# Kernel optimization log

Hardware: AMD Instinct MI355X
Metric: run time of the kernel (lower is better)

Reference implementation:

```python
import jax, jax.numpy as jnp
import numpy as np

B_SZ = 4; SEQ = 2048; D_INPUT = 40; D_MODEL = 128; N_LAYERS = 4
D_STATE = 16; EXPAND = 2; D_INNER = D_MODEL * EXPAND
N_HEADS = 4; D_HEAD = D_MODEL // N_HEADS; MAX_LANDMARKS = 100
EPS_RMS = 1.1920929e-07  # torch nn.RMSNorm default eps = finfo(float32).eps
EPS_LN = 1e-5
A_FLOOR = 1e-4


def _rms(x, w):
    return x * jax.lax.rsqrt(jnp.mean(x * x, -1, keepdims=True) + EPS_RMS) * w


def _ln(x, w, b):
    m = jnp.mean(x, -1, keepdims=True)
    v = jnp.mean((x - m) ** 2, -1, keepdims=True)
    return (x - m) * jax.lax.rsqrt(v + EPS_LN) * w + b


def _mamba3_block(xin, Wi, Wx, Wdt, bdt, Alog, Bb, Cb, Bnw, Cnw, rf, Dv, Wo):
    # xin: (B,L,d_model)
    xz = xin @ Wi                       # (B,L,2*d_inner)
    xp, z = jnp.split(xz, 2, axis=-1)
    xp = jax.nn.silu(xp)
    sp = xp @ Wx                        # (B,L,2*d_state+2)
    B_raw = sp[..., :D_STATE]
    C_raw = sp[..., D_STATE:2 * D_STATE]
    dt_in = sp[..., -2:-1]
    lam_in = sp[..., -1:]
    Bm = _rms(B_raw + Bb, Bnw)
    Cm = _rms(C_raw + Cb, Cnw)
    dt = jax.nn.softplus(dt_in @ Wdt + bdt)   # (B,L,d_inner)
    lam = jax.nn.sigmoid(lam_in)              # (B,L,1)
    # data-dependent RoPE on B and C
    freqs = jax.nn.softplus(rf)                                  # (d_state//2,)
    ang = jnp.cumsum(jnp.mean(dt, -1, keepdims=True), axis=1) * freqs  # (B,L,ds/2)
    ca, sa = jnp.cos(ang), jnp.sin(ang)

    def rot(M):
        e, o = M[..., ::2], M[..., 1::2]
        return jnp.stack([e * ca - o * sa, e * sa + o * ca], -1).reshape(M.shape)

    Bm, Cm = rot(Bm), rot(Cm)
    A = jnp.minimum(-jnp.exp(Alog), -A_FLOOR)   # (d_inner,d_state)
    dte = dt[..., None]                          # (B,L,d_inner,1)
    dA = jnp.exp(A * dte)                        # (B,L,d_inner,d_state)
    Bx = Bm[:, :, None, :] * xp[..., None]       # (B,L,d_inner,d_state)
    Bx_prev = jnp.concatenate([jnp.zeros_like(Bx[:, :1]), Bx[:, :-1]], axis=1)
    lame = lam[..., None]                        # (B,L,1,1)
    u = (1.0 - lame) * dte * dA * Bx_prev + lame * dte * Bx
    u = u.at[:, 0].set(dte[:, 0] * Bx[:, 0])     # t==0 case: h = dt*B*x (no lambda)

    def step(h, inp):
        dA_t, u_t, C_t = inp
        h = dA_t * h + u_t
        return h, jnp.sum(h * C_t[:, None, :], -1)

    h0 = jnp.zeros((xin.shape[0], D_INNER, D_STATE), xin.dtype)
    _, ys = jax.lax.scan(step, h0, (jnp.swapaxes(dA, 0, 1), jnp.swapaxes(u, 0, 1), jnp.swapaxes(Cm, 0, 1)))
    y = jnp.swapaxes(ys, 0, 1)                   # (B,L,d_inner)
    y = y + xp * Dv
    y = y * jax.nn.silu(z)
    return y @ Wo


def _landmark_attn(mo, skip, hw, WQ, bQ, WK, bK, WV, bV, WO, bO):
    Bsz, L, Dm = skip.shape
    k = min(MAX_LANDMARKS, L)
    _, idx = jax.lax.top_k(hw, k)
    idx = jnp.sort(idx, axis=1)                            # (B,k)
    kv = jnp.take_along_axis(skip, idx[..., None], axis=1)  # (B,k,Dm)
    q = mo[:, -1:, :]                                       # (B,1,Dm)
    Q = (q @ WQ + bQ).reshape(Bsz, 1, N_HEADS, D_HEAD).transpose(0, 2, 1, 3)
    K = (kv @ WK + bK).reshape(Bsz, k, N_HEADS, D_HEAD).transpose(0, 2, 1, 3)
    V = (kv @ WV + bV).reshape(Bsz, k, N_HEADS, D_HEAD).transpose(0, 2, 1, 3)
    scores = jnp.einsum('bhqd,bhkd->bhqk', Q, K) * (D_HEAD ** -0.5)
    probs = jax.nn.softmax(scores, axis=-1)
    out = jnp.einsum('bhqk,bhkd->bhqd', probs, V).transpose(0, 2, 1, 3).reshape(Bsz, Dm)
    return out @ WO + bO


def setup_inputs() -> dict:
    key = jax.random.key(0)
    ks = iter(jax.random.split(key, 64))

    def nrm(shape, s=0.02):
        return jax.random.normal(next(ks), shape, jnp.float32) * s

    nl, ds, di, dm = N_LAYERS, D_STATE, D_INNER, D_MODEL
    inp = {}
    inp['x'] = jax.random.normal(next(ks), (B_SZ, SEQ, D_INPUT), jnp.float32)
    inp['hawkes_weights'] = jax.random.uniform(next(ks), (B_SZ, SEQ), jnp.float32)
    inp['emb_W'] = nrm((D_INPUT, dm)); inp['emb_b'] = jnp.zeros(dm, jnp.float32)
    inp['skip_W'] = nrm((D_INPUT, dm)); inp['skip_b'] = jnp.zeros(dm, jnp.float32)
    inp['in_proj_W'] = nrm((nl, dm, 2 * di))
    inp['x_proj_W'] = nrm((nl, di, 2 * ds + 2))
    inp['dt_proj_W'] = nrm((nl, 1, di), 1.0)
    inp['dt_proj_b'] = jnp.full((nl, di), -1.0, jnp.float32)
    inp['A_log'] = jnp.broadcast_to(jnp.log(jnp.arange(1, ds + 1, dtype=jnp.float32)), (nl, di, ds)) * jnp.ones((nl, di, ds), jnp.float32)
    inp['B_bias'] = jnp.ones((nl, ds), jnp.float32)
    inp['C_bias'] = jnp.ones((nl, ds), jnp.float32)
    inp['Bn_w'] = jnp.ones((nl, ds), jnp.float32)
    inp['Cn_w'] = jnp.ones((nl, ds), jnp.float32)
    inp['rope_freqs'] = nrm((nl, ds // 2), 0.01)
    inp['D_param'] = jnp.ones((nl, di), jnp.float32)
    inp['out_proj_W'] = nrm((nl, di, dm))
    inp['ln_w'] = jnp.ones((nl, dm), jnp.float32); inp['ln_b'] = jnp.zeros((nl, dm), jnp.float32)
    inp['fn_w'] = jnp.ones(dm, jnp.float32); inp['fn_b'] = jnp.zeros(dm, jnp.float32)
    for nm in ('Q', 'K', 'V', 'O'):
        inp['W' + nm] = nrm((dm, dm)); inp['b' + nm] = jnp.zeros(dm, jnp.float32)
    return inp


def reference(x, hawkes_weights, emb_W, emb_b, skip_W, skip_b, in_proj_W, x_proj_W,
              dt_proj_W, dt_proj_b, A_log, B_bias, C_bias, Bn_w, Cn_w, rope_freqs,
              D_param, out_proj_W, ln_w, ln_b, fn_w, fn_b, WQ, bQ, WK, bK, WV, bV, WO, bO):
    w = hawkes_weights[..., None]
    h = (x @ emb_W + emb_b) * w          # Hawkes-damped embedding for Mamba path
    skip = (x @ skip_W + skip_b) * w     # Hawkes skip for attention KV
    for i in range(N_LAYERS):
        h = h + _mamba3_block(_ln(h, ln_w[i], ln_b[i]), in_proj_W[i], x_proj_W[i],
                              dt_proj_W[i], dt_proj_b[i], A_log[i], B_bias[i], C_bias[i],
                              Bn_w[i], Cn_w[i], rope_freqs[i], D_param[i], out_proj_W[i])
    mo = _ln(h, fn_w, fn_b)
    return _landmark_attn(mo, skip, hawkes_weights, WQ, bQ, WK, bK, WV, bV, WO, bO)
```

## Files before the change

kernel.cpp:

```cpp
#include <hip/hip_runtime.h>
#include <hip/hip_fp16.h>
#include <math.h>

#define BSZ   4
#define SEQL  2048
#define DIN   40
#define DM    128
#define DI    256
#define DS    16
#define NL    4
#define NHEAD 4
#define DHEAD 32
#define KLM   100
#define NC    128
#define TC    16
#define NROWS 8
#define EROWS 16

typedef _Float16 v2h __attribute__((ext_vector_type(2)));

__device__ __forceinline__ float rcp_(float x){ return __builtin_amdgcn_rcpf(x); }
__device__ __forceinline__ float sigmoidf_(float x){ return rcp_(1.0f + __expf(-x)); }
__device__ __forceinline__ float siluf_(float x){ return x*rcp_(1.0f + __expf(-x)); }
__device__ __forceinline__ float softplusf_(float x){ return fmaxf(x,0.0f) + __logf(1.0f + __expf(-fabsf(x))); }
__device__ __forceinline__ float fdot2_(__half2 a, __half2 b, float c){
  return __builtin_amdgcn_fdot2(*(v2h*)&a, *(v2h*)&b, c, false);
}

__device__ __forceinline__ void load8(const float* p, float* r){
  const float4* q = (const float4*)p;
  float4 a=q[0], b=q[1];
  r[0]=a.x;r[1]=a.y;r[2]=a.z;r[3]=a.w; r[4]=b.x;r[5]=b.y;r[6]=b.z;r[7]=b.w;
}
__device__ __forceinline__ void store8(float* p, const float* r){
  float4* q = (float4*)p;
  q[0]=make_float4(r[0],r[1],r[2],r[3]);  q[1]=make_float4(r[4],r[5],r[6],r[7]);
}
__device__ __forceinline__ void load16(const float* p, float* r){
  load8(p, r); load8(p+8, r+8);
}
__device__ __forceinline__ void store16(float* p, const float* r){
  store8(p, r); store8(p+8, r+8);
}

__global__ __launch_bounds__(256) void convw_kernel(
    const float* __restrict__ inW, const float* __restrict__ outW,
    __half* __restrict__ Wip, __half* __restrict__ Woh)
{
  const int i = blockIdx.x*256 + threadIdx.x;
  if (i < NL*DM*2*DI){
    const int col = i & 511;
    const int klin = i >> 9;
    const int l = klin >> 7, k = klin & 127;
    Wip[(((size_t)(l*64 + (k>>1))*512 + col) << 1) + (k & 1)] = __float2half_rn(inW[i]);
  }
  if (i < NL*DI*DM) Woh[i] = __float2half_rn(outW[i]);
}

__global__ __launch_bounds__(256) void topk_kernel(
    const float* __restrict__ hw, int* __restrict__ idxl_g)
{
  __shared__ int redcnt[2][4];
  __shared__ int eqc[8][4], gtc[8][4];

  const int b = blockIdx.x;
  const int t = threadIdx.x;
  const int lane = t & 63, w = t >> 6;

  const float* hwp = hw + (size_t)b*SEQL;
  unsigned vb[8];
  #pragma unroll
  for (int q=0;q<8;q++) vb[q] = __float_as_uint(hwp[q*256 + t]);

  unsigned kth = 0u;
  for (int bit=31; bit>=0; --bit){
    const unsigned cand = kth | (1u << bit);
    int c0 = 0;
    #pragma unroll
    for (int q=0;q<8;q++) c0 += __popcll(__ballot(vb[q] >= cand));
    const int par = bit & 1;
    if (lane == 0) redcnt[par][w] = c0;
    __syncthreads();
    const int tot = redcnt[par][0]+redcnt[par][1]+redcnt[par][2]+redcnt[par][3];
    if (tot >= KLM) kth = cand;
  }

  unsigned long long beq[8], bgt[8];
  #pragma unroll
  for (int q=0;q<8;q++){
    beq[q] = __ballot(vb[q] == kth);
    bgt[q] = __ballot(vb[q] >  kth);
  }
  if (lane == 0){
    #pragma unroll
    for (int q=0;q<8;q++){ eqc[q][w] = __popcll(beq[q]); gtc[q][w] = __popcll(bgt[q]); }
  }
  __syncthreads();
  {
    int gtTot = 0;
    #pragma unroll
    for (int q=0;q<8;q++) gtTot += gtc[q][0]+gtc[q][1]+gtc[q][2]+gtc[q][3];
    const int need_eq = KLM - gtTot;
    const unsigned long long lmask = (lane==0) ? 0ull : ((~0ull) >> (64-lane));
    int eqPfx = 0, gtPfx = 0;
    #pragma unroll
    for (int q=0;q<8;q++){
      int eqWP = 0, gtWP = 0;
      for (int w2=0; w2<w; ++w2){ eqWP += eqc[q][w2]; gtWP += gtc[q][w2]; }
      const int eqBefore = eqPfx + eqWP + __popcll(beq[q] & lmask);
      const int gtBefore = gtPfx + gtWP + __popcll(bgt[q] & lmask);
      if (vb[q] > kth){
        const int pos = gtBefore + min(eqBefore, need_eq);
        if (pos < KLM) idxl_g[b*KLM + pos] = q*256 + t;
      } else if (vb[q] == kth && eqBefore < need_eq){
        const int pos = gtBefore + eqBefore;
        if (pos < KLM) idxl_g[b*KLM + pos] = q*256 + t;
      }
      eqPfx += eqc[q][0]+eqc[q][1]+eqc[q][2]+eqc[q][3];
      gtPfx += gtc[q][0]+gtc[q][1]+gtc[q][2]+gtc[q][3];
    }
  }
}

__global__ __launch_bounds__(256) void embed_kernel(
    const float* __restrict__ x, const float* __restrict__ hw,
    const float* __restrict__ eW, const float* __restrict__ eb,
    const float* __restrict__ sW, const float* __restrict__ sb,
    float* __restrict__ hb, float* __restrict__ sk)
{
  __shared__ float xr[EROWS][DIN];
  const int t = threadIdx.x;
  const size_t R0 = (size_t)blockIdx.x * EROWS;
  for (int e=t; e<EROWS*DIN; e+=256) ((float*)xr)[e] = x[R0*DIN + e];
  __syncthreads();
  const int c = t & (DM-1), g = t >> 7;
  float ae[8], as[8];
  #pragma unroll
  for (int j=0;j<8;j++){ ae[j]=0.0f; as[j]=0.0f; }
  for (int k=0;k<DIN;k++){
    const float we  = eW[(size_t)k*DM + c];
    const float ws_ = sW[(size_t)k*DM + c];
    #pragma unroll
    for (int j=0;j<8;j++){
      const float xv = xr[g*8+j][k];
      ae[j] = fmaf(xv, we, ae[j]);
      as[j] = fmaf(xv, ws_, as[j]);
    }
  }
  const float ebv = eb[c], sbv = sb[c];
  #pragma unroll
  for (int j=0;j<8;j++){
    const size_t R = R0 + g*8 + j;
    const float w = hw[R];
    hb[R*DM + c] = (ae[j]+ebv)*w;
    sk[R*DM + c] = (as[j]+sbv)*w;
  }
}

__global__ __launch_bounds__(256) void pre_kernel(
    const float* __restrict__ hb,
    const __half* __restrict__ Wip, const float* __restrict__ Wx,
    const float* __restrict__ Wdt, const float* __restrict__ bdt,
    const float* __restrict__ Bb, const float* __restrict__ Cb,
    const float* __restrict__ Bnw, const float* __restrict__ Cnw,
    const float* __restrict__ lnw, const float* __restrict__ lnb,
    __half* __restrict__ xph, __half* __restrict__ zsh,
    float* __restrict__ dtin, float* __restrict__ Shalf,
    float* __restrict__ Bmb, float* __restrict__ Cmb,
    float* __restrict__ lamb, float* __restrict__ mdtb)
{
  __shared__ __half2 xinh[NROWS][64+2];
  __shared__ float xps[NROWS][DI+4];
  __shared__ float spl[NROWS][40];
  __shared__ float pr[NROWS][4];

  const int t = threadIdx.x;
  const size_t R0 = (size_t)blockIdx.x * NROWS;

  {
    const int r = t >> 5, j = t & 31;
    const float4 v = ((const float4*)(hb + (R0 + r)*DM))[j];
    float s = v.x+v.y+v.z+v.w;
    #pragma unroll
    for (int o=16;o>0;o>>=1) s += __shfl_xor(s,o,32);
    const float m = s*(1.0f/DM);
    const float dx=v.x-m, dy=v.y-m, dz=v.z-m, dw=v.w-m;
    float ss = dx*dx+dy*dy+dz*dz+dw*dw;
    #pragma unroll
    for (int o=16;o>0;o>>=1) ss += __shfl_xor(ss,o,32);
    const float inv = 1.0f/sqrtf(ss*(1.0f/DM) + 1e-5f);
    const int c = j*4;
    const float v0 = dx*inv*lnw[c+0] + lnb[c+0];
    const float v1 = dy*inv*lnw[c+1] + lnb[c+1];
    const float v2 = dz*inv*lnw[c+2] + lnb[c+2];
    const float v3 = dw*inv*lnw[c+3] + lnb[c+3];
    xinh[r][2*j]   = __halves2half2(__float2half_rn(v0), __float2half_rn(v1));
    xinh[r][2*j+1] = __halves2half2(__float2half_rn(v2), __float2half_rn(v3));
  }
  __syncthreads();

  {
    float2 a[NROWS];
    #pragma unroll
    for (int r=0;r<NROWS;r++){ a[r].x=0.0f; a[r].y=0.0f; }
    const __half2* Wc = (const __half2*)Wip + 2*t;
    #pragma unroll 4
    for (int p=0;p<64;p++){
      const float2 wv = *(const float2*)&Wc[(size_t)p*512];
      const __half2 w0 = *(const __half2*)&wv.x;
      const __half2 w1 = *(const __half2*)&wv.y;
      #pragma unroll
      for (int r=0;r<NROWS;r++){
        const __half2 xv = xinh[r][p];
        a[r].x = fdot2_(xv, w0, a[r].x);
        a[r].y = fdot2_(xv, w1, a[r].y);
      }
    }
    if (t < 128){
      #pragma unroll
      for (int r=0;r<NROWS;r++){
        const float sx = siluf_(a[r].x), sy = siluf_(a[r].y);
        xps[r][2*t] = sx; xps[r][2*t+1] = sy;
        *(__half2*)&xph[(R0+r)*DI + 2*t] =
            __halves2half2(__float2half_rn(sx), __float2half_rn(sy));
      }
    } else {
      const int zc = 2*t - 2*DI + DI;
      #pragma unroll
      for (int r=0;r<NROWS;r++){
        const float sx = siluf_(a[r].x), sy = siluf_(a[r].y);
        *(__half2*)&zsh[(R0+r)*DI + zc] =
            __halves2half2(__float2half_rn(sx), __float2half_rn(sy));
      }
    }
  }
  __syncthreads();

  if (t < 136){
    const int r = t & 7, op = t >> 3;
    float ax=0.0f, ay=0.0f;
    for (int k=0;k<DI;k+=4){
      const float4 xv = *(const float4*)&xps[r][k];
      const float2 w0 = *(const float2*)&Wx[(size_t)(k+0)*34 + 2*op];
      const float2 w1 = *(const float2*)&Wx[(size_t)(k+1)*34 + 2*op];
      const float2 w2 = *(const float2*)&Wx[(size_t)(k+2)*34 + 2*op];
      const float2 w3 = *(const float2*)&Wx[(size_t)(k+3)*34 + 2*op];
      ax = fmaf(xv.x,w0.x,ax); ay = fmaf(xv.x,w0.y,ay);
      ax = fmaf(xv.y,w1.x,ax); ay = fmaf(xv.y,w1.y,ay);
      ax = fmaf(xv.z,w2.x,ax); ay = fmaf(xv.z,w2.y,ay);
      ax = fmaf(xv.w,w3.x,ax); ay = fmaf(xv.w,w3.y,ay);
    }
    spl[r][2*op] = ax; spl[r][2*op+1] = ay;
  }
  __syncthreads();

  {
    const int half = t >> 7;
    const int r2 = (t >> 4) & 7, s2 = t & 15;
    const float* bias = half ? Cb : Bb;
    const float* wn   = half ? Cnw : Bnw;
    const float v = spl[r2][half*DS + s2] + bias[s2];
    float ss = v*v;
    #pragma unroll
    for (int o=8;o>0;o>>=1) ss += __shfl_xor(ss,o,16);
    const float inv = 1.0f/sqrtf(ss*(1.0f/DS) + 1.1920929e-07f);
    (half ? Cmb : Bmb)[(R0+r2)*DS + s2] = v*inv*wn[s2];
  }

  {
    const int lane = t & 63, w = t >> 6;
    const float wdt = Wdt[t], bdtv = bdt[t];
    float Sd = 0.0f;
    #pragma unroll
    for (int r=0;r<NROWS;r++){
      const float dval = softplusf_(fmaf(spl[r][32], wdt, bdtv));
      Sd += dval;
      float s = dval;
      #pragma unroll
      for (int o=32;o>0;o>>=1) s += __shfl_xor(s,o,64);
      if (lane==0) pr[r][w] = s;
    }
    Shalf[(size_t)blockIdx.x * DI + t] = Sd;
    if (t < NROWS){
      lamb[R0+t] = sigmoidf_(spl[t][33]);
      dtin[R0+t] = spl[t][32];
    }
  }
  __syncthreads();
  if (t < NROWS)
    mdtb[R0+t] = (pr[t][0]+pr[t][1]+pr[t][2]+pr[t][3])*(1.0f/DI);
}

__global__ __launch_bounds__(256) void cumcs_kernel(
    const float* __restrict__ mdt, const float* __restrict__ rf,
    float2* __restrict__ cst)
{
  __shared__ double csum[SEQL];
  __shared__ double wsum[4];
  __shared__ double fqs[8];
  const int b = blockIdx.x, t = threadIdx.x;
  const int lane = t & 63, w = t >> 6;
  if (t < 8){
    const double xfr = (double)rf[t];
    fqs[t] = fmax(xfr, 0.0) + log1p(exp(-fabs(xfr)));
  }
  const float* p = mdt + (size_t)b*SEQL + (size_t)t*8;
  double v[8]; double s = 0.0;
  #pragma unroll
  for (int q=0;q<8;q++){ v[q] = (double)p[q]; s += v[q]; }
  double sc = s;
  #pragma unroll
  for (int o=1;o<64;o<<=1){
    const double nb = __shfl_up(sc, o, 64);
    if (lane >= o) sc += nb;
  }
  if (lane==63) wsum[w] = sc;
  __syncthreads();
  double woff = 0.0;
  for (int j=0;j<w;j++) woff += wsum[j];
  double run = woff + sc - s;
  #pragma unroll
  for (int q=0;q<8;q++){ run += v[q]; csum[t*8+q] = run; }
  __syncthreads();

  const double TWO_PI = 6.283185307179586;
  const double INV2PI = 0.15915494309189535;
  for (int j=0;j<8;j++){
    const int rloc = j*256 + t;
    const double ab = csum[rloc];
    float2 o8[8];
    #pragma unroll
    for (int f=0; f<8; f++){
      const double ang = ab * fqs[f];
      const double red = ang - floor(ang*INV2PI)*TWO_PI;
      float sa, ca;
      __sincosf((float)red, &sa, &ca);
      o8[f] = make_float2(ca, sa);
    }
    float4* dst = (float4*)&cst[((size_t)b*SEQL + rloc)*8];
    dst[0] = make_float4(o8[0].x,o8[0].y,o8[1].x,o8[1].y);
    dst[1] = make_float4(o8[2].x,o8[2].y,o8[3].x,o8[3].y);
    dst[2] = make_float4(o8[4].x,o8[4].y,o8[5].x,o8[5].y);
    dst[3] = make_float4(o8[6].x,o8[6].y,o8[7].x,o8[7].y);
  }
}

__global__ __launch_bounds__(512) void scan1_kernel(
    const __half* __restrict__ xph, const float* __restrict__ dtin,
    const float* __restrict__ Wdt, const float* __restrict__ bdt,
    const float* __restrict__ Bmb, const float* __restrict__ lamb,
    const float2* __restrict__ cst,
    const float* __restrict__ Alog, float* __restrict__ hend)
{
  __shared__ float Bst[TC+1][DS];
  __shared__ float lst[TC];
  __shared__ float dsl[TC];
  __shared__ __half xpl[TC+1][DI+8];
  const int t = threadIdx.x;
  const int d  = t >> 1;
  const int s0 = (t & 1) * 8;
  const int c = blockIdx.x & (NC-1);
  const int b = blockIdx.x >> 7;
  const size_t bL = (size_t)b*SEQL;
  const int t0 = c*TC;
  const int id = blockIdx.x*256 + d;

  for (int e=t; e<(TC+1)*DS; e+=512){
    const int j = e >> 4, s = e & 15;
    const int trow = t0 - 1 + j;
    Bst[j][s] = (trow >= 0) ? Bmb[(bL + trow)*DS + s] : 0.0f;
  }
  for (int e=t; e<(TC+1)*DI; e+=512){
    const int j = e >> 8, dd = e & (DI-1);
    const int trow = t0 - 1 + j;
    xpl[j][dd] = (trow >= 0) ? xph[(bL + trow)*DI + dd] : __float2half_rn(0.0f);
  }
  if (t < TC){
    lst[t] = lamb[bL + t0 + t];
    dsl[t] = dtin[bL + t0 + t];
  }
  __syncthreads();
  if (t < 136){
    const int j = t >> 3, f = t & 7;
    const int trow = t0 - 1 + j;
    if (trow >= 0){
      const float2 cs = cst[((size_t)(bL + trow))*8 + f];
      const float e0 = Bst[j][2*f], o0 = Bst[j][2*f+1];
      Bst[j][2*f]   = e0*cs.x - o0*cs.y;
      Bst[j][2*f+1] = e0*cs.y + o0*cs.x;
    }
  }
  __syncthreads();

  float A[8];
  #pragma unroll
  for (int s=0;s<8;s++) A[s] = fminf(-__expf(Alog[d*DS + s0 + s]), -1e-4f);
  const float wdt = Wdt[d], bdtv = bdt[d];
  float h[8], Bprev[8];
  #pragma unroll
  for (int s=0;s<8;s++) h[s]=0.0f;
  float xpm1;
  int tstart;
  if (t0 > 0){
    #pragma unroll
    for (int s=0;s<8;s++) Bprev[s] = Bst[0][s0+s];
    xpm1 = __half2float(xpl[0][d]);
    tstart = 0;
  } else {
    const float dtv = softplusf_(fmaf(dsl[0], wdt, bdtv));
    const float xpv = __half2float(xpl[1][d]);
    #pragma unroll
    for (int s=0;s<8;s++){
      h[s] = dtv*(Bst[1][s0+s]*xpv);
      Bprev[s] = Bst[1][s0+s];
    }
    xpm1 = xpv;
    tstart = 1;
  }
  for (int j=tstart; j<TC; ++j){
    const float dtv = softplusf_(fmaf(dsl[j], wdt, bdtv));
    const float xpv = __half2float(xpl[j+1][d]);
    const float lamv = lst[j];
    const float dl = dtv*lamv;
    const float dml = dtv - dl;
    #pragma unroll
    for (int s=0;s<8;s++){
      const float a = __expf(A[s]*dtv);
      const float Bc = Bst[j+1][s0+s];
      const float u = fmaf(dml*a, Bprev[s]*xpm1, dl*(Bc*xpv));
      h[s] = fmaf(a, h[s], u);
      Bprev[s] = Bc;
    }
    xpm1 = xpv;
  }
  store8(hend + (size_t)id*DS + s0, h);
}

__global__ __launch_bounds__(128) void scan2_kernel(
    float* __restrict__ hend, const float* __restrict__ Shalf,
    const float* __restrict__ Alog)
{
  __shared__ float hS[NC][DS+1];
  __shared__ float pS[NC][DS+1];
  const int c = threadIdx.x;
  const int d = blockIdx.x & (DI-1);
  const int b = blockIdx.x >> 8;
  const float S = Shalf[(size_t)(b*(SEQL/NROWS) + 2*c)*DI + d]
                + Shalf[(size_t)(b*(SEQL/NROWS) + 2*c + 1)*DI + d];
  float P[DS], h[DS];
  #pragma unroll
  for (int s=0;s<DS;s++){
    const float A = fminf(-__expf(Alog[d*DS+s]), -1e-4f);
    P[s] = __expf(A*S);
  }
  load16(hend + (((size_t)(b*NC + c))*DI + d)*DS, h);
  #pragma unroll
  for (int s=0;s<DS;s++){ hS[c][s]=h[s]; pS[c][s]=P[s]; }
  __syncthreads();
  for (int off=1; off<NC; off<<=1){
    float hn[DS], pn[DS];
    const int src = c - off;
    if (src >= 0){
      #pragma unroll
      for (int s=0;s<DS;s++){ hn[s]=hS[src][s]; pn[s]=pS[src][s]; }
    }
    __syncthreads();
    if (src >= 0){
      #pragma unroll
      for (int s=0;s<DS;s++){
        h[s] = fmaf(P[s], hn[s], h[s]);
        P[s] *= pn[s];
        hS[c][s] = h[s]; pS[c][s] = P[s];
      }
    }
    __syncthreads();
  }
  float o[DS];
  if (c == 0){
    #pragma unroll
    for (int s=0;s<DS;s++) o[s] = 0.0f;
  } else {
    #pragma unroll
    for (int s=0;s<DS;s++) o[s] = hS[c-1][s];
  }
  store16(hend + (((size_t)(b*NC + c))*DI + d)*DS, o);
}

__global__ __launch_bounds__(512) void scan3post_kernel(
    const __half* __restrict__ xph, const float* __restrict__ dtin,
    const float* __restrict__ Wdt, const float* __restrict__ bdt,
    const float* __restrict__ Bmb, const float* __restrict__ Cmb,
    const float* __restrict__ lamb, const __half* __restrict__ zsh,
    const float2* __restrict__ cst,
    const float* __restrict__ Alog, const float* __restrict__ Dv,
    const float* __restrict__ Hin, const __half* __restrict__ Woh,
    float* __restrict__ hb)
{
  __shared__ float Bst[TC+1][DS];
  __shared__ float Cst[TC][DS];
  __shared__ float lst[TC];
  __shared__ float dsl[TC];
  __shared__ __half xpl[TC+1][DI+8];
  __shared__ __half zsl[TC][DI+8];
  __shared__ float ys[TC][DI+4];
  const int t = threadIdx.x;
  const int d  = t >> 1;
  const int sh = t & 1;
  const int s0 = sh * 8;
  const int c = blockIdx.x & (NC-1);
  const int b = blockIdx.x >> 7;
  const size_t bL = (size_t)b*SEQL;
  const int t0 = c*TC;
  const int id = blockIdx.x*256 + d;

  for (int e=t; e<(TC+1)*DS; e+=512){
    const int j = e >> 4, s = e & 15;
    const int trow = t0 - 1 + j;
    Bst[j][s] = (trow >= 0) ? Bmb[(bL + trow)*DS + s] : 0.0f;
    if (j < TC) Cst[j][s] = Cmb[(bL + t0 + j)*DS + s];
  }
  for (int e=t; e<(TC+1)*DI; e+=512){
    const int j = e >> 8, dd = e & (DI-1);
    const int trow = t0 - 1 + j;
    xpl[j][dd] = (trow >= 0) ? xph[(bL + trow)*DI + dd] : __float2half_rn(0.0f);
    if (j < TC) zsl[j][dd] = zsh[(bL + t0 + j)*DI + dd];
  }
  if (t < TC){
    lst[t] = lamb[bL + t0 + t];
    dsl[t] = dtin[bL + t0 + t];
  }
  __syncthreads();
  if (t < 264){
    if (t < 136){
      const int j = t >> 3, f = t & 7;
      const int trow = t0 - 1 + j;
      if (trow >= 0){
        const float2 cs = cst[((size_t)(bL + trow))*8 + f];
        const float e0 = Bst[j][2*f], o0 = Bst[j][2*f+1];
        Bst[j][2*f]   = e0*cs.x - o0*cs.y;
        Bst[j][2*f+1] = e0*cs.y + o0*cs.x;
      }
    } else {
      const int e2 = t - 136;
      const int j = e2 >> 3, f = e2 & 7;
      const float2 cs = cst[((size_t)(bL + t0 + j))*8 + f];
      const float e0 = Cst[j][2*f], o0 = Cst[j][2*f+1];
      Cst[j][2*f]   = e0*cs.x - o0*cs.y;
      Cst[j][2*f+1] = e0*cs.y + o0*cs.x;
    }
  }
  __syncthreads();

  float A[8];
  #pragma unroll
  for (int s=0;s<8;s++) A[s] = fminf(-__expf(Alog[d*DS + s0 + s]), -1e-4f);
  const float wdt = Wdt[d], bdtv = bdt[d];
  const float dvp = Dv[d];
  float h[8], Bprev[8];
  load8(Hin + (size_t)id*DS + s0, h);
  float xpm1;
  int tstart;
  if (t0 > 0){
    #pragma unroll
    for (int s=0;s<8;s++) Bprev[s] = Bst[0][s0+s];
    xpm1 = __half2float(xpl[0][d]);
    tstart = 0;
  } else {
    const float dtv = softplusf_(fmaf(dsl[0], wdt, bdtv));
    const float xpv = __half2float(xpl[1][d]);
    float y = 0.0f;
    #pragma unroll
    for (int s=0;s<8;s++){
      h[s] = dtv*(Bst[1][s0+s]*xpv);
      y = fmaf(h[s], Cst[0][s0+s], y);
      Bprev[s] = Bst[1][s0+s];
    }
    const float ytot = y + __shfl_xor(y, 1, 64);
    if (sh == 0) ys[0][d] = (ytot + xpv*dvp)*__half2float(zsl[0][d]);
    xpm1 = xpv;
    tstart = 1;
  }
  for (int j=tstart; j<TC; ++j){
    const float dtv = softplusf_(fmaf(dsl[j], wdt, bdtv));
    const float xpv = __half2float(xpl[j+1][d]);
    const float lamv = lst[j];
    const float dl = dtv*lamv;
    const float dml = dtv - dl;
    float y = 0.0f;
    #pragma unroll
    for (int s=0;s<8;s++){
      const float a = __expf(A[s]*dtv);
      const float Bc = Bst[j+1][s0+s];
      const float u = fmaf(dml*a, Bprev[s]*xpm1, dl*(Bc*xpv));
      h[s] = fmaf(a, h[s], u);
      y = fmaf(h[s], Cst[j][s0+s], y);
      Bprev[s] = Bc;
    }
    const float ytot = y + __shfl_xor(y, 1, 64);
    if (sh == 0) ys[j][d] = (ytot + xpv*dvp)*__half2float(zsl[j][d]);
    xpm1 = xpv;
  }
  __syncthreads();

  {
    const int cg2  = t & 31;
    const int ks2  = (t >> 5) & 1;
    const int rg   = (t >> 6) & 3;
    const int ksHi = t >> 8;
    const int seg = ksHi*2 + ks2;
    const int k0 = seg*64;
    const int c0c = cg2*4;
    float acc[4][4];
    #pragma unroll
    for (int rr=0;rr<4;rr++){ acc[rr][0]=0.f; acc[rr][1]=0.f; acc[rr][2]=0.f; acc[rr][3]=0.f; }
    for (int k=k0; k<k0+64; k+=4){
      float4 yv[4];
      #pragma unroll
      for (int rr=0;rr<4;rr++) yv[rr] = *(const float4*)&ys[rg*4+rr][k];
      #pragma unroll
      for (int j=0;j<4;j++){
        const float2 wlo = __half22float2(*(const __half2*)&Woh[(size_t)(k+j)*DM + c0c]);
        const float2 whi = __half22float2(*(const __half2*)&Woh[(size_t)(k+j)*DM + c0c + 2]);
        const float y0 = (j==0)?yv[0].x:(j==1)?yv[0].y:(j==2)?yv[0].z:yv[0].w;
        const float y1 = (j==0)?yv[1].x:(j==1)?yv[1].y:(j==2)?yv[1].z:yv[1].w;
        const float y2 = (j==0)?yv[2].x:(j==1)?yv[2].y:(j==2)?yv[2].z:yv[2].w;
        const float y3 = (j==0)?yv[3].x:(j==1)?yv[3].y:(j==2)?yv[3].z:yv[3].w;
        acc[0][0]=fmaf(y0,wlo.x,acc[0][0]); acc[0][1]=fmaf(y0,wlo.y,acc[0][1]);
        acc[0][2]=fmaf(y0,whi.x,acc[0][2]); acc[0][3]=fmaf(y0,whi.y,acc[0][3]);
        acc[1][0]=fmaf(y1,wlo.x,acc[1][0]); acc[1][1]=fmaf(y1,wlo.y,acc[1][1]);
        acc[1][2]=fmaf(y1,whi.x,acc[1][2]); acc[1][3]=fmaf(y1,whi.y,acc[1][3]);
        acc[2][0]=fmaf(y2,wlo.x,acc[2][0]); acc[2][1]=fmaf(y2,wlo.y,acc[2][1]);
        acc[2][2]=fmaf(y2,whi.x,acc[2][2]); acc[2][3]=fmaf(y2,whi.y,acc[2][3]);
        acc[3][0]=fmaf(y3,wlo.x,acc[3][0]); acc[3][1]=fmaf(y3,wlo.y,acc[3][1]);
        acc[3][2]=fmaf(y3,whi.x,acc[3][2]); acc[3][3]=fmaf(y3,whi.y,acc[3][3]);
      }
    }
    #pragma unroll
    for (int rr=0;rr<4;rr++){
      #pragma unroll
      for (int cc=0;cc<4;cc++) acc[rr][cc] += __shfl_down(acc[rr][cc], 32, 64);
    }
    float (*red)[132] = (float(*)[132])ys;
    __syncthreads();
    const int lane = t & 63;
    if (ksHi == 1 && lane < 32){
      #pragma unroll
      for (int rr=0;rr<4;rr++)
        *(float4*)&red[rg*4+rr][c0c] = make_float4(acc[rr][0],acc[rr][1],acc[rr][2],acc[rr][3]);
    }
    __syncthreads();
    if (ksHi == 0 && lane < 32){
      #pragma unroll
      for (int rr=0;rr<4;rr++){
        const float4 rv = *(const float4*)&red[rg*4+rr][c0c];
        const size_t row = bL + t0 + rg*4 + rr;
        float4 hv = *(const float4*)&hb[row*DM + c0c];
        hv.x += acc[rr][0] + rv.x; hv.y += acc[rr][1] + rv.y;
        hv.z += acc[rr][2] + rv.z; hv.w += acc[rr][3] + rv.w;
        *(float4*)&hb[row*DM + c0c] = hv;
      }
    }
  }
}

__global__ __launch_bounds__(256) void attnmid_kernel(
    const float* __restrict__ hb, const float* __restrict__ sk,
    const int* __restrict__ idxl_g,
    const float* __restrict__ fnw, const float* __restrict__ fnb,
    const float* __restrict__ WQ, const float* __restrict__ bQ,
    const float* __restrict__ WK, const float* __restrict__ bK,
    const float* __restrict__ WV, const float* __restrict__ bV,
    float* __restrict__ attnog)
{
  __shared__ float kv[KLM][DM+4];
  __shared__ float mo[DM];
  __shared__ float Qs[DHEAD];
  __shared__ float qk[DM];
  __shared__ float sc[KLM];
  __shared__ float pbar[DM];
  __shared__ float bterm_s;
  const int t = threadIdx.x;
  const int b = blockIdx.x >> 2, hh = blockIdx.x & 3;
  const int c0 = hh*DHEAD;

  if (t < 64){
    const float* hr = hb + ((size_t)b*SEQL + (SEQL-1))*DM;
    const float v0 = hr[t], v1 = hr[t+64];
    float s = v0+v1;
    #pragma unroll
    for (int o=32;o>0;o>>=1) s += __shfl_xor(s,o,64);
    const float m = s*(1.0f/DM);
    const float d0=v0-m, d1=v1-m;
    float ss = d0*d0 + d1*d1;
    #pragma unroll
    for (int o=32;o>0;o>>=1) ss += __shfl_xor(ss,o,64);
    const float inv = 1.0f/sqrtf(ss*(1.0f/DM) + 1e-5f);
    mo[t]    = d0*inv*fnw[t]    + fnb[t];
    mo[t+64] = d1*inv*fnw[t+64] + fnb[t+64];
  }
  for (int e=t; e<KLM*DM; e+=256){
    const int j = e >> 7, cc = e & (DM-1);
    kv[j][cc] = sk[((size_t)b*SEQL + idxl_g[b*KLM + j])*DM + cc];
  }
  __syncthreads();
  if (t < DHEAD){
    float a = bQ[c0+t];
    #pragma unroll 4
    for (int k=0;k<DM;k++) a = fmaf(mo[k], WQ[(size_t)k*DM + c0+t], a);
    Qs[t] = a;
  }
  __syncthreads();
  if (t < DM){
    float a = 0.0f;
    #pragma unroll
    for (int cc=0; cc<DHEAD; cc++) a = fmaf(WK[(size_t)t*DM + c0 + cc], Qs[cc], a);
    qk[t] = a;
  } else if (t == DM){
    float a = 0.0f;
    for (int cc=0; cc<DHEAD; cc++) a += bK[c0+cc]*Qs[cc];
    bterm_s = a;
  }
  __syncthreads();
  if (t < KLM){
    float a = bterm_s;
    for (int m=0;m<DM;m+=4){
      const float4 kvv = *(const float4*)&kv[t][m];
      const float4 qv  = *(const float4*)&qk[m];
      a = fmaf(kvv.x,qv.x,a); a = fmaf(kvv.y,qv.y,a);
      a = fmaf(kvv.z,qv.z,a); a = fmaf(kvv.w,qv.w,a);
    }
    sc[t] = a*0.17677669529663687f;
  }
  __syncthreads();
  if (t < 64){
    const int lane = t;
    const float v0 = (lane < KLM) ? sc[lane] : -3.0e38f;
    const float v1 = (lane+64 < KLM) ? sc[lane+64] : -3.0e38f;
    float mx = fmaxf(v0, v1);
    #pragma unroll
    for (int o2=32;o2>0;o2>>=1) mx = fmaxf(mx, __shfl_xor(mx,o2,64));
    const float e0 = (lane < KLM) ? __expf(v0-mx) : 0.0f;
    const float e1 = (lane+64 < KLM) ? __expf(v1-mx) : 0.0f;
    float sm = e0+e1;
    #pragma unroll
    for (int o2=32;o2>0;o2>>=1) sm += __shfl_xor(sm,o2,64);
    const float inv2 = rcp_(sm);
    if (lane < KLM) sc[lane] = e0*inv2;
    if (lane+64 < KLM) sc[lane+64] = e1*inv2;
  }
  __syncthreads();
  if (t < DM){
    float a = 0.0f;
    #pragma unroll 4
    for (int j=0;j<KLM;j++) a = fmaf(sc[j], kv[j][t], a);
    pbar[t] = a;
  }
  __syncthreads();
  if (t < DHEAD){
    const int cc = c0 + t;
    float a = bV[cc];
    #pragma unroll 4
    for (int m=0;m<DM;m++) a = fmaf(pbar[m], WV[(size_t)m*DM + cc], a);
    attnog[b*DM + cc] = a;
  }
}

__global__ __launch_bounds__(128) void attnout_kernel(
    const float* __restrict__ attnog, const float* __restrict__ WO,
    const float* __restrict__ bO, float* __restrict__ outp)
{
  __shared__ float ao[DM];
  const int b = blockIdx.x, t = threadIdx.x;
  ao[t] = attnog[b*DM + t];
  __syncthreads();
  float a = bO[t];
  #pragma unroll 4
  for (int c2=0;c2<DM;c2++) a = fmaf(ao[c2], WO[(size_t)c2*DM + t], a);
  outp[(size_t)b*DM + t] = a;
}

extern "C" void kernel_launch(void* const* d_in, const int* in_sizes, int n_in,
                              void* d_out, int out_size, void* d_ws, size_t ws_size,
                              hipStream_t stream)
{
  (void)in_sizes; (void)n_in; (void)out_size; (void)ws_size;
  const float* x    = (const float*)d_in[0];
  const float* hw   = (const float*)d_in[1];
  const float* embW = (const float*)d_in[2];
  const float* embB = (const float*)d_in[3];
  const float* skW  = (const float*)d_in[4];
  const float* skB  = (const float*)d_in[5];
  const float* inW  = (const float*)d_in[6];
  const float* xpW  = (const float*)d_in[7];
  const float* dtW  = (const float*)d_in[8];
  const float* dtB  = (const float*)d_in[9];
  const float* Alog = (const float*)d_in[10];
  const float* Bb   = (const float*)d_in[11];
  const float* Cb   = (const float*)d_in[12];
  const float* Bnw  = (const float*)d_in[13];
  const float* Cnw  = (const float*)d_in[14];
  const float* rf   = (const float*)d_in[15];
  const float* Dpar = (const float*)d_in[16];
  const float* outW = (const float*)d_in[17];
  const float* lnW  = (const float*)d_in[18];
  const float* lnB  = (const float*)d_in[19];
  const float* fnW  = (const float*)d_in[20];
  const float* fnB  = (const float*)d_in[21];
  const float* WQ = (const float*)d_in[22]; const float* bQ = (const float*)d_in[23];
  const float* WK = (const float*)d_in[24]; const float* bK = (const float*)d_in[25];
  const float* WV = (const float*)d_in[26]; const float* bV = (const float*)d_in[27];
  const float* WO = (const float*)d_in[28]; const float* bO = (const float*)d_in[29];

  float* ws = (float*)d_ws;
  size_t off = 0;
  float* hb    = ws + off; off += (size_t)BSZ*SEQL*DM;
  float* sk    = ws + off; off += (size_t)BSZ*SEQL*DM;
  __half* xph  = (__half*)(ws + off); off += (size_t)BSZ*SEQL*DI/2;
  __half* zsh  = (__half*)(ws + off); off += (size_t)BSZ*SEQL*DI/2;
  float* Bmb   = ws + off; off += (size_t)BSZ*SEQL*DS;
  float* Cmb   = ws + off; off += (size_t)BSZ*SEQL*DS;
  float* lamb  = ws + off; off += (size_t)BSZ*SEQL;
  float* mdtb  = ws + off; off += (size_t)BSZ*SEQL;
  float* dtin  = ws + off; off += (size_t)BSZ*SEQL;
  float* Shalf = ws + off; off += (size_t)BSZ*(SEQL/NROWS)*DI;
  float* hend  = ws + off; off += (size_t)BSZ*NC*DI*DS;
  float2* cst  = (float2*)(ws + off); off += (size_t)BSZ*SEQL*16;
  int* idxl_g  = (int*)(ws + off); off += (size_t)BSZ*KLM;
  float* attnog= ws + off; off += (size_t)BSZ*DM;
  __half* Wip  = (__half*)(ws + off); off += (size_t)NL*DM*2*DI/2;
  __half* Woh  = (__half*)(ws + off); off += (size_t)NL*DI*DM/2;

  convw_kernel<<<(NL*DM*2*DI + 255)/256, 256, 0, stream>>>(inW, outW, Wip, Woh);
  topk_kernel<<<BSZ, 256, 0, stream>>>(hw, idxl_g);
  embed_kernel<<<BSZ*SEQL/EROWS, 256, 0, stream>>>(x, hw, embW, embB, skW, skB, hb, sk);

  for (int i=0;i<NL;i++){
    pre_kernel<<<BSZ*SEQL/NROWS, 256, 0, stream>>>(hb,
        Wip + (size_t)i*DM*2*DI, xpW + (size_t)i*DI*34,
        dtW + (size_t)i*DI, dtB + (size_t)i*DI,
        Bb + i*DS, Cb + i*DS, Bnw + i*DS, Cnw + i*DS,
        lnW + i*DM, lnB + i*DM,
        xph, zsh, dtin, Shalf, Bmb, Cmb, lamb, mdtb);
    cumcs_kernel<<<BSZ, 256, 0, stream>>>(mdtb, rf + i*8, cst);
    scan1_kernel<<<BSZ*NC, 512, 0, stream>>>(xph, dtin,
        dtW + (size_t)i*DI, dtB + (size_t)i*DI,
        Bmb, lamb, cst, Alog + (size_t)i*DI*DS, hend);
    scan2_kernel<<<BSZ*DI, 128, 0, stream>>>(hend, Shalf, Alog + (size_t)i*DI*DS);
    scan3post_kernel<<<BSZ*NC, 512, 0, stream>>>(xph, dtin,
        dtW + (size_t)i*DI, dtB + (size_t)i*DI,
        Bmb, Cmb, lamb, zsh, cst,
        Alog + (size_t)i*DI*DS, Dpar + (size_t)i*DI, hend,
        Woh + (size_t)i*DI*DM, hb);
  }

  attnmid_kernel<<<BSZ*NHEAD, 256, 0, stream>>>(hb, sk, idxl_g, fnW, fnB,
      WQ, bQ, WK, bK, WV, bV, attnog);
  attnout_kernel<<<BSZ, 128, 0, stream>>>(attnog, WO, bO, (float*)d_out);
}
```

Baseline: 507.4 us.

## Compute RoPE sincos inside scan kernels and use fp16 dot2 out-projection

The cumulative-sum kernel now only writes the double-precision prefix sums. The RoPE cos/sin evaluation moves into scan1 and scan3post, which recompute it per chunk instead of reading a precomputed table. This removes the serial sincos work from a 4-block kernel and the table traffic, at the cost of repeated double math and sincos in every chunk block. Separately, the out-projection weights are repacked as k-pairs and y is stored in fp16, so the out-projection uses fdot2 with half the shared memory. That lowers precision of the y activations.

```diff
diff --git a/kernel.cpp b/kernel.cpp
--- a/kernel.cpp
+++ b/kernel.cpp
@@ -45,7 +45,7 @@
 
 __global__ __launch_bounds__(256) void convw_kernel(
     const float* __restrict__ inW, const float* __restrict__ outW,
-    __half* __restrict__ Wip, __half* __restrict__ Woh)
+    __half* __restrict__ Wip, __half* __restrict__ Wop)
 {
   const int i = blockIdx.x*256 + threadIdx.x;
   if (i < NL*DM*2*DI){
@@ -54,7 +54,12 @@
     const int l = klin >> 7, k = klin & 127;
     Wip[(((size_t)(l*64 + (k>>1))*512 + col) << 1) + (k & 1)] = __float2half_rn(inW[i]);
   }
-  if (i < NL*DI*DM) Woh[i] = __float2half_rn(outW[i]);
+  if (i < NL*DI*DM){
+    const int c = i & (DM-1);
+    const int klin = i >> 7;
+    const int l = klin >> 8, k = klin & 255;
+    Wop[(((size_t)(l*128 + (k>>1))*DM + c) << 1) + (k & 1)] = __float2half_rn(outW[i]);
+  }
 }
 
 __global__ __launch_bounds__(256) void topk_kernel(
@@ -291,19 +296,12 @@
     mdtb[R0+t] = (pr[t][0]+pr[t][1]+pr[t][2]+pr[t][3])*(1.0f/DI);
 }
 
-__global__ __launch_bounds__(256) void cumcs_kernel(
-    const float* __restrict__ mdt, const float* __restrict__ rf,
-    float2* __restrict__ cst)
-{
-  __shared__ double csum[SEQL];
+__global__ __launch_bounds__(256) void cumsum_kernel(
+    const float* __restrict__ mdt, double* __restrict__ csum_g)
+{
   __shared__ double wsum[4];
-  __shared__ double fqs[8];
   const int b = blockIdx.x, t = threadIdx.x;
   const int lane = t & 63, w = t >> 6;
-  if (t < 8){
-    const double xfr = (double)rf[t];
-    fqs[t] = fmax(xfr, 0.0) + log1p(exp(-fabs(xfr)));
-  }
   const float* p = mdt + (size_t)b*SEQL + (size_t)t*8;
   double v[8]; double s = 0.0;
   #pragma unroll
@@ -319,42 +317,22 @@
   double woff = 0.0;
   for (int j=0;j<w;j++) woff += wsum[j];
   double run = woff + sc - s;
-  #pragma unroll
-  for (int q=0;q<8;q++){ run += v[q]; csum[t*8+q] = run; }
-  __syncthreads();
-
-  const double TWO_PI = 6.283185307179586;
-  const double INV2PI = 0.15915494309189535;
-  for (int j=0;j<8;j++){
-    const int rloc = j*256 + t;
-    const double ab = csum[rloc];
-    float2 o8[8];
-    #pragma unroll
-    for (int f=0; f<8; f++){
-      const double ang = ab * fqs[f];
-      const double red = ang - floor(ang*INV2PI)*TWO_PI;
-      float sa, ca;
-      __sincosf((float)red, &sa, &ca);
-      o8[f] = make_float2(ca, sa);
-    }
-    float4* dst = (float4*)&cst[((size_t)b*SEQL + rloc)*8];
-    dst[0] = make_float4(o8[0].x,o8[0].y,o8[1].x,o8[1].y);
-    dst[1] = make_float4(o8[2].x,o8[2].y,o8[3].x,o8[3].y);
-    dst[2] = make_float4(o8[4].x,o8[4].y,o8[5].x,o8[5].y);
-    dst[3] = make_float4(o8[6].x,o8[6].y,o8[7].x,o8[7].y);
-  }
+  double* dst = csum_g + (size_t)b*SEQL + (size_t)t*8;
+  #pragma unroll
+  for (int q=0;q<8;q++){ run += v[q]; dst[q] = run; }
 }
 
 __global__ __launch_bounds__(512) void scan1_kernel(
     const __half* __restrict__ xph, const float* __restrict__ dtin,
     const float* __restrict__ Wdt, const float* __restrict__ bdt,
     const float* __restrict__ Bmb, const float* __restrict__ lamb,
-    const float2* __restrict__ cst,
+    const double* __restrict__ csum_g, const float* __restrict__ rf,
     const float* __restrict__ Alog, float* __restrict__ hend)
 {
   __shared__ float Bst[TC+1][DS];
   __shared__ float lst[TC];
   __shared__ float dsl[TC];
+  __shared__ double fqs[8];
   __shared__ __half xpl[TC+1][DI+8];
   const int t = threadIdx.x;
   const int d  = t >> 1;
@@ -365,6 +343,10 @@
   const int t0 = c*TC;
   const int id = blockIdx.x*256 + d;
 
+  if (t < 8){
+    const double xfr = (double)rf[t];
+    fqs[t] = fmax(xfr, 0.0) + log1p(exp(-fabs(xfr)));
+  }
   for (int e=t; e<(TC+1)*DS; e+=512){
     const int j = e >> 4, s = e & 15;
     const int trow = t0 - 1 + j;
@@ -384,10 +366,13 @@
     const int j = t >> 3, f = t & 7;
     const int trow = t0 - 1 + j;
     if (trow >= 0){
-      const float2 cs = cst[((size_t)(bL + trow))*8 + f];
+      const double ang = csum_g[bL + trow] * fqs[f];
+      const double red = ang - floor(ang*0.15915494309189535)*6.283185307179586;
+      float sa, ca;
+      __sincosf((float)red, &sa, &ca);
       const float e0 = Bst[j][2*f], o0 = Bst[j][2*f+1];
-      Bst[j][2*f]   = e0*cs.x - o0*cs.y;
-      Bst[j][2*f+1] = e0*cs.y + o0*cs.x;
+      Bst[j][2*f]   = e0*ca - o0*sa;
+      Bst[j][2*f+1] = e0*sa + o0*ca;
     }
   }
   __syncthreads();
@@ -491,18 +476,20 @@
     const float* __restrict__ Wdt, const float* __restrict__ bdt,
     const float* __restrict__ Bmb, const float* __restrict__ Cmb,
     const float* __restrict__ lamb, const __half* __restrict__ zsh,
-    const float2* __restrict__ cst,
+    const double* __restrict__ csum_g, const float* __restrict__ rf,
     const float* __restrict__ Alog, const float* __restrict__ Dv,
-    const float* __restrict__ Hin, const __half* __restrict__ Woh,
+    const float* __restrict__ Hin, const __half* __restrict__ Wop,
     float* __restrict__ hb)
 {
   __shared__ float Bst[TC+1][DS];
   __shared__ float Cst[TC][DS];
   __shared__ float lst[TC];
   __shared__ float dsl[TC];
+  __shared__ double fqs[8];
   __shared__ __half xpl[TC+1][DI+8];
   __shared__ __half zsl[TC][DI+8];
-  __shared__ float ys[TC][DI+4];
+  __shared__ __half ysh[TC][DI+8];
+  __shared__ float red[TC][132];
   const int t = threadIdx.x;
   const int d  = t >> 1;
   const int sh = t & 1;
@@ -513,6 +500,10 @@
   const int t0 = c*TC;
   const int id = blockIdx.x*256 + d;
 
+  if (t < 8){
+    const double xfr = (double)rf[t];
+    fqs[t] = fmax(xfr, 0.0) + log1p(exp(-fabs(xfr)));
+  }
   for (int e=t; e<(TC+1)*DS; e+=512){
     const int j = e >> 4, s = e & 15;
     const int trow = t0 - 1 + j;
@@ -535,18 +526,24 @@
       const int j = t >> 3, f = t & 7;
       const int trow = t0 - 1 + j;
       if (trow >= 0){
-        const float2 cs = cst[((size_t)(bL + trow))*8 + f];
+        const double ang = csum_g[bL + trow] * fqs[f];
+        const double rd = ang - floor(ang*0.15915494309189535)*6.283185307179586;
+        float sa, ca;
+        __sincosf((float)rd, &sa, &ca);
         const float e0 = Bst[j][2*f], o0 = Bst[j][2*f+1];
-        Bst[j][2*f]   = e0*cs.x - o0*cs.y;
-        Bst[j][2*f+1] = e0*cs.y + o0*cs.x;
+        Bst[j][2*f]   = e0*ca - o0*sa;
+        Bst[j][2*f+1] = e0*sa + o0*ca;
       }
     } else {
       const int e2 = t - 136;
       const int j = e2 >> 3, f = e2 & 7;
-      const float2 cs = cst[((size_t)(bL + t0 + j))*8 + f];
+      const double ang = csum_g[bL + t0 + j] * fqs[f];
+      const double rd = ang - floor(ang*0.15915494309189535)*6.283185307179586;
+      float sa, ca;
+      __sincosf((float)rd, &sa, &ca);
       const float e0 = Cst[j][2*f], o0 = Cst[j][2*f+1];
-      Cst[j][2*f]   = e0*cs.x - o0*cs.y;
-      Cst[j][2*f+1] = e0*cs.y + o0*cs.x;
+      Cst[j][2*f]   = e0*ca - o0*sa;
+      Cst[j][2*f+1] = e0*sa + o0*ca;
     }
   }
   __syncthreads();
@@ -576,7 +573,7 @@
       Bprev[s] = Bst[1][s0+s];
     }
     const float ytot = y + __shfl_xor(y, 1, 64);
-    if (sh == 0) ys[0][d] = (ytot + xpv*dvp)*__half2float(zsl[0][d]);
+    if (sh == 0) ysh[0][d] = __float2half_rn((ytot + xpv*dvp)*__half2float(zsl[0][d]));
     xpm1 = xpv;
     tstart = 1;
   }
@@ -597,7 +594,7 @@
       Bprev[s] = Bc;
     }
     const float ytot = y + __shfl_xor(y, 1, 64);
-    if (sh == 0) ys[j][d] = (ytot + xpv*dvp)*__half2float(zsl[j][d]);
+    if (sh == 0) ysh[j][d] = __float2half_rn((ytot + xpv*dvp)*__half2float(zsl[j][d]));
     xpm1 = xpv;
   }
   __syncthreads();
@@ -608,31 +605,26 @@
     const int rg   = (t >> 6) & 3;
     const int ksHi = t >> 8;
     const int seg = ksHi*2 + ks2;
-    const int k0 = seg*64;
+    const int k0p = seg*32;
     const int c0c = cg2*4;
+    const __half2* Wp = (const __half2*)Wop;
     float acc[4][4];
     #pragma unroll
     for (int rr=0;rr<4;rr++){ acc[rr][0]=0.f; acc[rr][1]=0.f; acc[rr][2]=0.f; acc[rr][3]=0.f; }
-    for (int k=k0; k<k0+64; k+=4){
-      float4 yv[4];
-      #pragma unroll
-      for (int rr=0;rr<4;rr++) yv[rr] = *(const float4*)&ys[rg*4+rr][k];
-      #pragma unroll
-      for (int j=0;j<4;j++){
-        const float2 wlo = __half22float2(*(const __half2*)&Woh[(size_t)(k+j)*DM + c0c]);
-        const float2 whi = __half22float2(*(const __half2*)&Woh[(size_t)(k+j)*DM + c0c + 2]);
-        const float y0 = (j==0)?yv[0].x:(j==1)?yv[0].y:(j==2)?yv[0].z:yv[0].w;
-        const float y1 = (j==0)?yv[1].x:(j==1)?yv[1].y:(j==2)?yv[1].z:yv[1].w;
-        const float y2 = (j==0)?yv[2].x:(j==1)?yv[2].y:(j==2)?yv[2].z:yv[2].w;
-        const float y3 = (j==0)?yv[3].x:(j==1)?yv[3].y:(j==2)?yv[3].z:yv[3].w;
-        acc[0][0]=fmaf(y0,wlo.x,acc[0][0]); acc[0][1]=fmaf(y0,wlo.y,acc[0][1]);
-        acc[0][2]=fmaf(y0,whi.x,acc[0][2]); acc[0][3]=fmaf(y0,whi.y,acc[0][3]);
-        acc[1][0]=fmaf(y1,wlo.x,acc[1][0]); acc[1][1]=fmaf(y1,wlo.y,acc[1][1]);
-        acc[1][2]=fmaf(y1,whi.x,acc[1][2]); acc[1][3]=fmaf(y1,whi.y,acc[1][3]);
-        acc[2][0]=fmaf(y2,wlo.x,acc[2][0]); acc[2][1]=fmaf(y2,wlo.y,acc[2][1]);
-        acc[2][2]=fmaf(y2,whi.x,acc[2][2]); acc[2][3]=fmaf(y2,whi.y,acc[2][3]);
-        acc[3][0]=fmaf(y3,wlo.x,acc[3][0]); acc[3][1]=fmaf(y3,wlo.y,acc[3][1]);
-        acc[3][2]=fmaf(y3,whi.x,acc[3][2]); acc[3][3]=fmaf(y3,whi.y,acc[3][3]);
+    for (int kp=k0p; kp<k0p+32; ++kp){
+      const float2 wv0 = *(const float2*)&Wp[(size_t)kp*DM + c0c];
+      const float2 wv1 = *(const float2*)&Wp[(size_t)kp*DM + c0c + 2];
+      const __half2 wc0 = *(const __half2*)&wv0.x;
+      const __half2 wc1 = *(const __half2*)&wv0.y;
+      const __half2 wc2 = *(const __half2*)&wv1.x;
+      const __half2 wc3 = *(const __half2*)&wv1.y;
+      #pragma unroll
+      for (int rr=0;rr<4;rr++){
+        const __half2 yv = *(const __half2*)&ysh[rg*4+rr][2*kp];
+        acc[rr][0] = fdot2_(yv, wc0, acc[rr][0]);
+        acc[rr][1] = fdot2_(yv, wc1, acc[rr][1]);
+        acc[rr][2] = fdot2_(yv, wc2, acc[rr][2]);
+        acc[rr][3] = fdot2_(yv, wc3, acc[rr][3]);
       }
     }
     #pragma unroll
@@ -640,7 +632,6 @@
       #pragma unroll
       for (int cc=0;cc<4;cc++) acc[rr][cc] += __shfl_down(acc[rr][cc], 32, 64);
     }
-    float (*red)[132] = (float(*)[132])ys;
     __syncthreads();
     const int lane = t & 63;
     if (ksHi == 1 && lane < 32){
@@ -824,13 +815,13 @@
   float* dtin  = ws + off; off += (size_t)BSZ*SEQL;
   float* Shalf = ws + off; off += (size_t)BSZ*(SEQL/NROWS)*DI;
   float* hend  = ws + off; off += (size_t)BSZ*NC*DI*DS;
-  float2* cst  = (float2*)(ws + off); off += (size_t)BSZ*SEQL*16;
+  double* csum_g = (double*)(ws + off); off += (size_t)BSZ*SEQL*2;
   int* idxl_g  = (int*)(ws + off); off += (size_t)BSZ*KLM;
   float* attnog= ws + off; off += (size_t)BSZ*DM;
   __half* Wip  = (__half*)(ws + off); off += (size_t)NL*DM*2*DI/2;
-  __half* Woh  = (__half*)(ws + off); off += (size_t)NL*DI*DM/2;
-
-  convw_kernel<<<(NL*DM*2*DI + 255)/256, 256, 0, stream>>>(inW, outW, Wip, Woh);
+  __half* Wop  = (__half*)(ws + off); off += (size_t)NL*DI*DM/2;
+
+  convw_kernel<<<(NL*DM*2*DI + 255)/256, 256, 0, stream>>>(inW, outW, Wip, Wop);
   topk_kernel<<<BSZ, 256, 0, stream>>>(hw, idxl_g);
   embed_kernel<<<BSZ*SEQL/EROWS, 256, 0, stream>>>(x, hw, embW, embB, skW, skB, hb, sk);
 
@@ -841,16 +832,16 @@
         Bb + i*DS, Cb + i*DS, Bnw + i*DS, Cnw + i*DS,
         lnW + i*DM, lnB + i*DM,
         xph, zsh, dtin, Shalf, Bmb, Cmb, lamb, mdtb);
-    cumcs_kernel<<<BSZ, 256, 0, stream>>>(mdtb, rf + i*8, cst);
+    cumsum_kernel<<<BSZ, 256, 0, stream>>>(mdtb, csum_g);
     scan1_kernel<<<BSZ*NC, 512, 0, stream>>>(xph, dtin,
         dtW + (size_t)i*DI, dtB + (size_t)i*DI,
-        Bmb, lamb, cst, Alog + (size_t)i*DI*DS, hend);
+        Bmb, lamb, csum_g, rf + i*8, Alog + (size_t)i*DI*DS, hend);
     scan2_kernel<<<BSZ*DI, 128, 0, stream>>>(hend, Shalf, Alog + (size_t)i*DI*DS);
     scan3post_kernel<<<BSZ*NC, 512, 0, stream>>>(xph, dtin,
         dtW + (size_t)i*DI, dtB + (size_t)i*DI,
-        Bmb, Cmb, lamb, zsh, cst,
+        Bmb, Cmb, lamb, zsh, csum_g, rf + i*8,
         Alog + (size_t)i*DI*DS, Dpar + (size_t)i*DI, hend,
-        Woh + (size_t)i*DI*DM, hb);
+        Wop + (size_t)i*DI*DM, hb);
   }
 
   attnmid_kernel<<<BSZ*NHEAD, 256, 0, stream>>>(hb, sk, idxl_g, fnW, fnB,
```

Result: faster. 496.7 us (-2.1%).
